# Kernel optimization log

Hardware: AMD Instinct MI355X
Metric: run time of the kernel (lower is better)

## Reference

```python
import jax, jax.numpy as jnp
import numpy as np

H, DK, DV, CHUNK = 4, 256, 256, 32

def _silu(x):
    return x * jax.nn.sigmoid(x)

def _l2norm(x, eps=1e-6):
    return x * jax.lax.rsqrt(jnp.sum(x * x, -1, keepdims=True) + eps)

def _rmsnorm(x, w, eps=1e-5):
    return x * jax.lax.rsqrt(jnp.mean(x * x, -1, keepdims=True) + eps) * w

def _causal_dwconv(x, w):
    # x: (B, L, C), w: (C, K) -> causal depthwise conv -> (B, L, C)
    C = x.shape[-1]
    K = w.shape[-1]
    xp = jnp.pad(x, ((0, 0), (K - 1, 0), (0, 0))).transpose(0, 2, 1)  # NCH
    y = jax.lax.conv_general_dilated(xp, w[:, None, :], (1,), 'VALID',
                                     feature_group_count=C,
                                     dimension_numbers=('NCH', 'OIH', 'NCH'))
    return y.transpose(0, 2, 1)

def _fir(x, filt):
    # x: (B, L, H, D), filt: (H, D, K) depthwise causal FIR per (head, channel)
    B, L, h, d = x.shape
    y = _causal_dwconv(x.reshape(B, L, h * d), filt.reshape(h * d, -1))
    return y.reshape(B, L, h, d)

def _delta_rule_chunkwise(q, k, v, beta):
    # q,k: (B,H,L,DK); v: (B,H,L,DV); beta: (B,H,L). L % CHUNK == 0.
    b, h, L, dk = q.shape
    dv = v.shape[-1]
    n = L // CHUNK
    q = _l2norm(q)
    k = _l2norm(k)
    v = v * beta[..., None]
    k_beta = k * beta[..., None]
    rs = lambda t: t.reshape(b, h, n, CHUNK, -1)
    q, k, v, k_beta = rs(q), rs(k), rs(v), rs(k_beta)
    eye = jnp.eye(CHUNK, dtype=q.dtype)
    strict_lower = jnp.tril(jnp.ones((CHUNK, CHUNK), bool), -1)
    A = jnp.where(strict_lower, jnp.einsum('bhncd,bhnsd->bhncs', k_beta, k), 0.0)
    # The torch row-wise loop computes (I + strict_lower(K_beta K^T))^{-1}
    attn_inv = jax.scipy.linalg.solve_triangular(eye + A, jnp.broadcast_to(eye, A.shape), lower=True)
    u = attn_inv @ v       # (b,h,n,c,dv)
    w = attn_inv @ k_beta  # (b,h,n,c,dk)
    incl_lower = jnp.tril(jnp.ones((CHUNK, CHUNK), bool))

    def step(S, inp):
        q_i, k_i, u_i, w_i = inp
        attn_local = jnp.where(incl_lower, q_i @ jnp.swapaxes(k_i, -1, -2), 0.0)
        u_t = u_i - w_i @ S
        o_i = q_i @ S + attn_local @ u_t
        return S + jnp.swapaxes(k_i, -1, -2) @ u_t, o_i

    S0 = jnp.zeros((b, h, dk, dv), q.dtype)
    xs = tuple(jnp.moveaxis(t, 2, 0) for t in (q, k, u, w))
    S, out = jax.lax.scan(step, S0, xs)
    return jnp.moveaxis(out, 0, 2).reshape(b, h, L, dv), S

def _stats(x):
    # per-branch head statistics over feature dim: mean, var, abs-mean, l2-norm
    return jnp.stack([x.mean(-1), x.var(-1), jnp.abs(x).mean(-1),
                      jnp.sqrt(jnp.sum(x * x, -1))], -1)

def _forward(x, Wq, Wk, Wv, Wb, conv_q, conv_k, conv_v, fir_long, fir_short,
             W1, b1, W2, b2, log_temp, base_bias, conv_residual_logit, rms_w, Wo):
    B, L, D = x.shape
    q = _silu(_causal_dwconv(x @ Wq, conv_q)).reshape(B, L, H, DK)
    k = _silu(_causal_dwconv(x @ Wk, conv_k)).reshape(B, L, H, DK)
    v = _silu(_causal_dwconv(x @ Wv, conv_v)).reshape(B, L, H, DV)
    beta = jax.nn.sigmoid(x @ Wb)  # (B, L, H)
    delta, _S = _delta_rule_chunkwise(q.transpose(0, 2, 1, 3), k.transpose(0, 2, 1, 3),
                                      v.transpose(0, 2, 1, 3), beta.transpose(0, 2, 1))
    delta = delta.transpose(0, 2, 1, 3)  # (B, L, H, DV)
    f_short = _fir(v, fir_short)
    f_long = _fir(v, fir_long)
    stats = jnp.concatenate([_stats(f_short), _stats(f_long), _stats(delta), _stats(v)], -1)
    hidden_exp = jnp.broadcast_to(x[:, :, None, :], (B, L, H, D))
    gate_in = jnp.concatenate([hidden_exp, stats], -1)  # (B,L,H,D+16)
    h1 = jax.nn.gelu(gate_in @ W1 + b1, approximate=False)
    logits = h1 @ W2 + b2 + base_bias  # (B, L, H, 4)
    temp = jax.nn.softplus(log_temp) + 1e-4
    p = jax.nn.softmax(logits / temp[:, None], -1)
    eps = 0.05  # step 0 -> alpha = 1 -> floor = floor_start
    p = jnp.maximum(p, jnp.array([eps, eps, 0.0, 0.0], p.dtype))
    p = p / jnp.sum(p, -1, keepdims=True)
    o = (p[..., 0:1] * f_short + p[..., 1:2] * f_long +
         p[..., 2:3] * delta + p[..., 3:4] * v)
    o = o + 0.5 * jax.nn.sigmoid(conv_residual_logit)[None, None, :, None] * f_short
    o = _rmsnorm(o, rms_w)
    return o.reshape(B, L, H * DV) @ Wo

def setup_inputs():
    key = jax.random.key(0)
    ks = jax.random.split(key, 13)
    B, L, D = 2, 2048, 1024
    f = jnp.float32
    n = lambda k, shape, s=0.02: jax.random.normal(k, shape, f) * s
    return {
        'x': jax.random.normal(ks[0], (B, L, D), f),
        'Wq': n(ks[1], (D, D)),
        'Wk': n(ks[2], (D, D)),
        'Wv': n(ks[3], (D, D)),
        'Wb': n(ks[4], (D, H)),
        'conv_q': n(ks[5], (D, 4), 0.1),
        'conv_k': n(ks[6], (D, 4), 0.1),
        'conv_v': n(ks[7], (D, 4), 0.1),
        'fir_long': n(ks[8], (H, DV, 64)),
        'fir_short': n(ks[9], (H, DV, 5)),
        'W1': n(ks[10], (D + 16, D)),
        'b1': jnp.zeros((D,), f),
        'W2': n(ks[11], (D, 4)),
        'b2': jnp.zeros((4,), f),
        'log_temp': jnp.full((H,), float(np.log(np.expm1(0.7))), f),
        'base_bias': jnp.tile(jnp.array([-0.5, -0.5, 1.0, 3.0], f), (H, 1)),
        'conv_residual_logit': jnp.full((H,), -2.0, f),
        'rms_w': jnp.ones((DV,), f),
        'Wo': n(ks[12], (D, D)),
    }

def reference(x, Wq, Wk, Wv, Wb, conv_q, conv_k, conv_v, fir_long, fir_short,
              W1, b1, W2, b2, log_temp, base_bias, conv_residual_logit, rms_w, Wo):
    return _forward(x, Wq, Wk, Wv, Wb, conv_q, conv_k, conv_v, fir_long, fir_short,
                    W1, b1, W2, b2, log_temp, base_bias, conv_residual_logit, rms_w, Wo)
```

## Files before the change

### kernel.cpp

```cpp
#include <hip/hip_runtime.h>
#include <math.h>

constexpr int NB = 2, NL = 2048, ND = 1024, NH = 4;
constexpr int NCHK = 64;
constexpr int NBL = NB * NL;
#define BLDSZ (NB * NL * ND)

constexpr int OPS_CH = 36864;
constexpr int STG_CH = 26624;

__device__ float g_q[BLDSZ];
__device__ float g_k[BLDSZ];
__device__ float g_v[BLDSZ];
__device__ float g_delta[BLDSZ];
__device__ float g_fs[BLDSZ];
__device__ float g_fl[BLDSZ];
__device__ float g_xw1[BLDSZ];
__device__ float g_beta[NBL * NH];
__device__ unsigned short g_ops[(size_t)8 * 64 * OPS_CH];
__device__ unsigned short g_xb[BLDSZ];
__device__ unsigned short g_omixb[BLDSZ];
__device__ unsigned short g_btw[5 * 1024 * 1024];

__device__ __forceinline__ float sigmoidf(float x) { return 1.f / (1.f + expf(-x)); }

__device__ __forceinline__ unsigned short f2bf(float f) {
  union { float f; unsigned int u; } v; v.f = f;
  unsigned int r = v.u + 0x7FFFu + ((v.u >> 16) & 1u);
  return (unsigned short)(r >> 16);
}
__device__ __forceinline__ float bf2f(unsigned int bits16) {
  union { unsigned int u; float f; } v; v.u = bits16 << 16; return v.f;
}
__device__ __forceinline__ unsigned int packbf(float a, float b) {
  return (unsigned int)f2bf(a) | ((unsigned int)f2bf(b) << 16);
}

typedef __attribute__((ext_vector_type(8))) short short8v;
typedef __attribute__((ext_vector_type(16))) float f32x16;

__device__ __forceinline__ unsigned int cvtpk(float lo, float hi) {
  unsigned int r;
  asm("v_cvt_pk_bf16_f32 %0, %1, %2" : "=v"(r) : "v"(lo), "v"(hi));
  return r;
}

__device__ __forceinline__ void mkfrag(const f32x16 v, short8v& fb0, short8v& fb1) {
  unsigned int P0 = cvtpk(v[0], v[1]),   P1 = cvtpk(v[2], v[3]);
  unsigned int P2 = cvtpk(v[4], v[5]),   P3 = cvtpk(v[6], v[7]);
  unsigned int P4 = cvtpk(v[8], v[9]),   P5 = cvtpk(v[10], v[11]);
  unsigned int P6 = cvtpk(v[12], v[13]), P7 = cvtpk(v[14], v[15]);
  asm("v_permlane32_swap_b32 %0, %1" : "+v"(P0), "+v"(P2));
  asm("v_permlane32_swap_b32 %0, %1" : "+v"(P1), "+v"(P3));
  asm("v_permlane32_swap_b32 %0, %1" : "+v"(P4), "+v"(P6));
  asm("v_permlane32_swap_b32 %0, %1" : "+v"(P5), "+v"(P7));
  unsigned int f0[4] = {P0, P1, P2, P3}, f1[4] = {P4, P5, P6, P7};
  fb0 = *(short8v*)f0; fb1 = *(short8v*)f1;
}

#define GLL16(SRC, DST)                                                                    \
  __builtin_amdgcn_global_load_lds(                                                        \
      (const __attribute__((address_space(1))) unsigned int*)(SRC),                        \
      (__attribute__((address_space(3))) unsigned int*)(DST), 16, 0, 0)

__device__ __forceinline__ void gemm128s(const unsigned short* __restrict__ A,
                                         const unsigned short* __restrict__ Bt,
                                         float* __restrict__ C, int m0, int n0, int t,
                                         unsigned short* As, unsigned short* Bs) {
  const int w = t >> 6, lane = t & 63, l31 = lane & 31, lhi = lane >> 5;
  const int wm = (w & 1) * 64, wn = (w >> 1) * 64;
  f32x16 acc[2][2];
#pragma unroll
  for (int mt = 0; mt < 2; ++mt)
#pragma unroll
    for (int nt = 0; nt < 2; ++nt)
#pragma unroll
      for (int e = 0; e < 16; ++e) acc[mt][nt][e] = 0.f;

  for (int k0 = 0; k0 < 1024; k0 += 32) {
    for (int sl = w; sl < 8; sl += 4) {
      int srow = sl * 16 + (lane >> 2);
      int gc = ((lane & 3) ^ (srow & 3)) * 8;
      GLL16(A + (size_t)(m0 + srow) * 1024 + k0 + gc, &As[sl * 512]);
      GLL16(Bt + (size_t)(n0 + srow) * 1024 + k0 + gc, &Bs[sl * 512]);
    }
    __syncthreads();
#pragma unroll
    for (int ksl = 0; ksl < 2; ++ksl) {
      int kb = ksl * 2 + lhi;
      short8v af[2], bf[2];
#pragma unroll
      for (int mt = 0; mt < 2; ++mt) {
        int row = wm + mt * 32 + l31;
        af[mt] = *(const short8v*)&As[row * 32 + ((kb ^ (row & 3)) * 8)];
      }
#pragma unroll
      for (int nt = 0; nt < 2; ++nt) {
        int row = wn + nt * 32 + l31;
        bf[nt] = *(const short8v*)&Bs[row * 32 + ((kb ^ (row & 3)) * 8)];
      }
#pragma unroll
      for (int mt = 0; mt < 2; ++mt)
#pragma unroll
        for (int nt = 0; nt < 2; ++nt)
          acc[mt][nt] = __builtin_amdgcn_mfma_f32_32x32x16_bf16(af[mt], bf[nt], acc[mt][nt], 0, 0, 0);
    }
    __syncthreads();
  }
#pragma unroll
  for (int mt = 0; mt < 2; ++mt)
#pragma unroll
    for (int nt = 0; nt < 2; ++nt) {
      int col = n0 + wn + nt * 32 + l31;
#pragma unroll
      for (int e = 0; e < 16; ++e) {
        int row = m0 + wm + mt * 32 + (e & 3) + 8 * (e >> 2) + 4 * lhi;
        C[(size_t)row * 1024 + col] = acc[mt][nt][e];
      }
    }
}

__global__ __launch_bounds__(256) void pack_all_kernel(const float* __restrict__ x,
                                                       const float* __restrict__ Wq,
                                                       const float* __restrict__ Wk,
                                                       const float* __restrict__ Wv,
                                                       const float* __restrict__ W1,
                                                       const float* __restrict__ Wo,
                                                       const float* __restrict__ Wb) {
  __shared__ float tile[64][65];
  int blk = blockIdx.x, t = threadIdx.x;
  if (blk < 2048) {
    int i8 = blk * 256 + t;
    const float* p = x + (size_t)i8 * 8;
    float4 a = *(const float4*)p;
    float4 b = *(const float4*)(p + 4);
    uint4 v;
    v.x = packbf(a.x, a.y); v.y = packbf(a.z, a.w);
    v.z = packbf(b.x, b.y); v.w = packbf(b.z, b.w);
    *(uint4*)&g_xb[(size_t)i8 * 8] = v;
    return;
  }
  if (blk < 3328) {
    int sel = (blk - 2048) >> 8, wb = (blk - 2048) & 255;
    const float* W = (sel == 0) ? Wq : (sel == 1) ? Wk : (sel == 2) ? Wv : (sel == 3) ? W1 : Wo;
    int bx = wb & 15, by = wb >> 4;
    int n0 = bx * 64, k0 = by * 64;
#pragma unroll
    for (int i = 0; i < 4; ++i) {
      int id = t + i * 256;
      int r = id >> 4, c4 = (id & 15) * 4;
      float4 v = *(const float4*)&W[(size_t)(k0 + r) * 1024 + n0 + c4];
      tile[r][c4 + 0] = v.x; tile[r][c4 + 1] = v.y; tile[r][c4 + 2] = v.z; tile[r][c4 + 3] = v.w;
    }
    __syncthreads();
    unsigned int* out = (unsigned int*)g_btw + (size_t)sel * 524288;
#pragma unroll
    for (int i = 0; i < 8; ++i) {
      int id = t + i * 256;
      int nn = id >> 5, ku = id & 31;
      out[(size_t)(n0 + nn) * 512 + (k0 >> 1) + ku] = packbf(tile[2 * ku][nn], tile[2 * ku + 1][nn]);
    }
    return;
  }
  int bl = blk - 3328;
  int h = t >> 6, lane = t & 63;
  const float* xr = x + (size_t)bl * ND;
  float acc = 0.f;
  for (int d = lane; d < ND; d += 64) acc += xr[d] * Wb[d * 4 + h];
#pragma unroll
  for (int off = 32; off; off >>= 1) acc += __shfl_xor(acc, off);
  if (lane == 0) g_beta[bl * 4 + h] = sigmoidf(acc);
}

__global__ __launch_bounds__(256, 3) void qkv_conv_kernel(const float* __restrict__ cq,
                                                          const float* __restrict__ ck,
                                                          const float* __restrict__ cv) {
  __shared__ unsigned short As[160 * 32];
  __shared__ unsigned short Bs[128 * 32];
  __shared__ unsigned short TF[131][132];
  const int sel = blockIdx.x >> 8, hb = blockIdx.x & 255;
  const unsigned short* A = g_xb;
  const unsigned short* Bt = g_btw + (size_t)sel * 1024 * 1024;
  const float* cw = (sel == 0) ? cq : (sel == 1) ? ck : cv;
  float* OUT = (sel == 0) ? g_q : (sel == 1) ? g_k : g_v;
  const int m0 = (hb >> 3) * 128, n0 = (hb & 7) * 128;
  const int t = threadIdx.x;
  const int w = t >> 6, lane = t & 63, l31 = lane & 31, lhi = lane >> 5;
  const int wm = (w & 1) * 64, wn = (w >> 1) * 64;

  f32x16 acc[2][2], acch;
#pragma unroll
  for (int mt = 0; mt < 2; ++mt)
#pragma unroll
    for (int nt = 0; nt < 2; ++nt)
#pragma unroll
      for (int e = 0; e < 16; ++e) acc[mt][nt][e] = 0.f;
#pragma unroll
  for (int e = 0; e < 16; ++e) acch[e] = 0.f;

  for (int k0 = 0; k0 < 1024; k0 += 32) {
    for (int sl = w; sl < 10; sl += 4) {
      int srow = sl * 16 + (lane >> 2);
      int gc = ((lane & 3) ^ (srow & 3)) * 8;
      int grow = m0 - 32 + srow;
      if (grow < 0) grow = 0;
      GLL16(A + (size_t)grow * 1024 + k0 + gc, &As[sl * 512]);
    }
    for (int sl = w; sl < 8; sl += 4) {
      int srow = sl * 16 + (lane >> 2);
      int gc = ((lane & 3) ^ (srow & 3)) * 8;
      GLL16(Bt + (size_t)(n0 + srow) * 1024 + k0 + gc, &Bs[sl * 512]);
    }
    __syncthreads();
#pragma unroll
    for (int ksl = 0; ksl < 2; ++ksl) {
      int kb = ksl * 2 + lhi;
      short8v af[2], bf[2], afh;
#pragma unroll
      for (int mt = 0; mt < 2; ++mt) {
        int row = 32 + wm + mt * 32 + l31;
        af[mt] = *(const short8v*)&As[row * 32 + ((kb ^ (row & 3)) * 8)];
      }
      {
        int row = l31;
        afh = *(const short8v*)&As[row * 32 + ((kb ^ (row & 3)) * 8)];
      }
#pragma unroll
      for (int nt = 0; nt < 2; ++nt) {
        int row = wn + nt * 32 + l31;
        bf[nt] = *(const short8v*)&Bs[row * 32 + ((kb ^ (row & 3)) * 8)];
      }
#pragma unroll
      for (int mt = 0; mt < 2; ++mt)
#pragma unroll
        for (int nt = 0; nt < 2; ++nt)
          acc[mt][nt] = __builtin_amdgcn_mfma_f32_32x32x16_bf16(af[mt], bf[nt], acc[mt][nt], 0, 0, 0);
      acch = __builtin_amdgcn_mfma_f32_32x32x16_bf16(afh, bf[w & 1], acch, 0, 0, 0);
    }
    __syncthreads();
  }

#pragma unroll
  for (int mt = 0; mt < 2; ++mt)
#pragma unroll
    for (int nt = 0; nt < 2; ++nt) {
      int tc = wn + nt * 32 + l31;
#pragma unroll
      for (int e = 0; e < 16; ++e) {
        int row_e = (e & 3) + 8 * (e >> 2) + 4 * lhi;
        TF[3 + wm + mt * 32 + row_e][tc] = f2bf(acc[mt][nt][e]);
      }
    }
#pragma unroll
  for (int e = 0; e < 16; ++e) {
    int row_e = (e & 3) + 8 * (e >> 2) + 4 * lhi;
    if (row_e >= 29) TF[row_e - 29][w * 32 + l31] = f2bf(acch[e]);
  }
  __syncthreads();

  {
    int c = t & 127;
    int rbase = (t >> 7) * 64;
    int ch = n0 + c;
    float w0 = cw[ch * 4 + 0], w1 = cw[ch * 4 + 1], w2 = cw[ch * 4 + 2], w3 = cw[ch * 4 + 3];
#pragma unroll 4
    for (int i = 0; i < 64; ++i) {
      int rr = rbase + i;
      int grow = m0 + rr;
      int l = grow & (NL - 1);
      float a = w3 * bf2f(TF[rr + 3][c]);
      if (l >= 1) a += w2 * bf2f(TF[rr + 2][c]);
      if (l >= 2) a += w1 * bf2f(TF[rr + 1][c]);
      if (l >= 3) a += w0 * bf2f(TF[rr + 0][c]);
      OUT[(size_t)grow * 1024 + ch] = a * sigmoidf(a);
    }
  }
}

__global__ __launch_bounds__(256) void hgemm_out_kernel(float* __restrict__ Cext) {
  __shared__ unsigned short As[128 * 32];
  __shared__ unsigned short Bs[128 * 32];
  gemm128s(g_omixb, g_btw + (size_t)4 * 1024 * 1024, Cext,
           (blockIdx.x >> 3) * 128, (blockIdx.x & 7) * 128, threadIdx.x, As, Bs);
}

__global__ __launch_bounds__(256) void delta_prep_kernel() {
  __shared__ float X[32][260];
  __shared__ float Y[32][260];
  __shared__ float Am[32][33];
  __shared__ float Tm[32][33];
  __shared__ float bet[32];
  int blk = blockIdx.x;
  int n = blk & 63, h = (blk >> 6) & 3, b = blk >> 8;
  int t = threadIdx.x;
  size_t rowbase = (size_t)(b * NL + n * 32);
  size_t obase = (size_t)blk * OPS_CH;
  const int st_ = t >> 5, j_ = (t >> 4) & 1, lh_ = (t >> 3) & 1, e_ = t & 7;
  const int l31_ = t & 31;

#pragma unroll
  for (int i = 0; i < 8; ++i) {
    int j = t + i * 256;
    int r = j >> 6, d4 = (j & 63) << 2;
    size_t gi = (rowbase + r) * ND + h * 256 + d4;
    *(float4*)&X[r][d4] = *(const float4*)&g_q[gi];
    *(float4*)&Y[r][d4] = *(const float4*)&g_k[gi];
  }
  if (t < 32) bet[t] = g_beta[(rowbase + t) * 4 + h];
  __syncthreads();

  {
    int wv = t >> 6, lane = t & 63;
    int r = wv * 8 + (lane >> 3), sub = lane & 7;
    float sq = 0.f, sk = 0.f;
#pragma unroll
    for (int m4 = 0; m4 < 8; ++m4) {
      float4 a = *(const float4*)&X[r][sub * 32 + m4 * 4];
      float4 bb = *(const float4*)&Y[r][sub * 32 + m4 * 4];
      sq += a.x * a.x + a.y * a.y + a.z * a.z + a.w * a.w;
      sk += bb.x * bb.x + bb.y * bb.y + bb.z * bb.z + bb.w * bb.w;
    }
    sq += __shfl_xor(sq, 1); sq += __shfl_xor(sq, 2); sq += __shfl_xor(sq, 4);
    sk += __shfl_xor(sk, 1); sk += __shfl_xor(sk, 2); sk += __shfl_xor(sk, 4);
    float rq = rsqrtf(sq + 1e-6f), rk = rsqrtf(sk + 1e-6f);
#pragma unroll
    for (int m4 = 0; m4 < 8; ++m4) {
      float4 a = *(const float4*)&X[r][sub * 32 + m4 * 4];
      a.x *= rq; a.y *= rq; a.z *= rq; a.w *= rq;
      *(float4*)&X[r][sub * 32 + m4 * 4] = a;
      float4 bb = *(const float4*)&Y[r][sub * 32 + m4 * 4];
      bb.x *= rk; bb.y *= rk; bb.z *= rk; bb.w *= rk;
      *(float4*)&Y[r][sub * 32 + m4 * 4] = bb;
    }
  }
  __syncthreads();

  if (t < 64) {
    const int al = t & 31, ah = t >> 5;
    f32x16 Cat;
#pragma unroll
    for (int e = 0; e < 16; ++e) Cat[e] = 0.f;
#pragma unroll
    for (int st = 0; st < 16; ++st) {
      int kb = st * 16 + ah * 8;
      float4 a0 = *(const float4*)&X[al][kb], a1 = *(const float4*)&X[al][kb + 4];
      float4 b0 = *(const float4*)&Y[al][kb], b1 = *(const float4*)&Y[al][kb + 4];
      unsigned int af[4] = {cvtpk(a0.x, a0.y), cvtpk(a0.z, a0.w), cvtpk(a1.x, a1.y), cvtpk(a1.z, a1.w)};
      unsigned int bf_[4] = {cvtpk(b0.x, b0.y), cvtpk(b0.z, b0.w), cvtpk(b1.x, b1.y), cvtpk(b1.z, b1.w)};
      Cat = __builtin_amdgcn_mfma_f32_32x32x16_bf16(*(short8v*)af, *(short8v*)bf_, Cat, 0, 0, 0);
    }
#pragma unroll
    for (int e = 0; e < 16; ++e) {
      int row = (e & 3) + 8 * (e >> 2) + 4 * ah, col = al;
      float v = (col <= row) ? Cat[e] : 0.f;
      g_ops[obase + 32768 + (size_t)(((col >> 4) * 64) + ((col >> 3) & 1) * 32 + row) * 8 + (col & 7)] = f2bf(v);
    }
  }

  {
    size_t qb = obase + 8192 + (size_t)(((st_ * 2 + j_) * 64) + lh_ * 32) * 8 + e_;
#pragma unroll 8
    for (int r = 0; r < 32; ++r)
      g_ops[qb + r * 8] = f2bf(X[r][t]);
#pragma unroll
    for (int j = 0; j < 2; ++j)
#pragma unroll
      for (int lh = 0; lh < 2; ++lh) {
        int kr0 = j * 16 + lh * 8;
        uint4 v;
        v.x = packbf(Y[kr0 + 0][t], Y[kr0 + 1][t]);
        v.y = packbf(Y[kr0 + 2][t], Y[kr0 + 3][t]);
        v.z = packbf(Y[kr0 + 4][t], Y[kr0 + 5][t]);
        v.w = packbf(Y[kr0 + 6][t], Y[kr0 + 7][t]);
        *(uint4*)&g_ops[obase + 16384 + (size_t)(((st_ * 2 + j) * 64) + lh * 32 + l31_) * 8] = v;
      }
  }
  __syncthreads();

#pragma unroll
  for (int i = 0; i < 8; ++i) {
    int j = t + i * 256;
    int r = j >> 6, d4 = (j & 63) << 2;
    float be = bet[r];
    float4 bb = *(const float4*)&Y[r][d4];
    bb.x *= be; bb.y *= be; bb.z *= be; bb.w *= be;
    *(float4*)&X[r][d4] = bb;
  }
  __syncthreads();

  if (t < 64) {
    const int al = t & 31, ah = t >> 5;
    f32x16 Cam;
#pragma unroll
    for (int e = 0; e < 16; ++e) Cam[e] = 0.f;
#pragma unroll
    for (int st = 0; st < 16; ++st) {
      int kb = st * 16 + ah * 8;
      float4 a0 = *(const float4*)&X[al][kb], a1 = *(const float4*)&X[al][kb + 4];
      float4 b0 = *(const float4*)&Y[al][kb], b1 = *(const float4*)&Y[al][kb + 4];
      unsigned int af[4] = {cvtpk(a0.x, a0.y), cvtpk(a0.z, a0.w), cvtpk(a1.x, a1.y), cvtpk(a1.z, a1.w)};
      unsigned int bf_[4] = {cvtpk(b0.x, b0.y), cvtpk(b0.z, b0.w), cvtpk(b1.x, b1.y), cvtpk(b1.z, b1.w)};
      Cam = __builtin_amdgcn_mfma_f32_32x32x16_bf16(*(short8v*)af, *(short8v*)bf_, Cam, 0, 0, 0);
    }
#pragma unroll
    for (int e = 0; e < 16; ++e) {
      int row = (e & 3) + 8 * (e >> 2) + 4 * ah, col = al;
      if (col < row) Am[row][col] = Cam[e];
    }
  }
  __syncthreads();

  if (t < 32) {
    int j = t;
    for (int i = 0; i < 32; ++i) {
      float a = (i == j) ? 1.f : 0.f;
      for (int m = j; m < i; ++m) a -= Am[i][m] * Tm[m][j];
      Tm[i][j] = a;
    }
  }
  __syncthreads();

  {
    float acc[32];
#pragma unroll
    for (int r = 0; r < 32; ++r) acc[r] = 0.f;
#pragma unroll
    for (int m = 0; m < 32; ++m) {
      float xv = X[m][t];
#pragma unroll
      for (int r = m; r < 32; ++r) acc[r] += Tm[r][m] * xv;
    }
    size_t wb = obase + (size_t)(((st_ * 2 + j_) * 64) + lh_ * 32) * 8 + e_;
#pragma unroll 8
    for (int r = 0; r < 32; ++r)
      g_ops[wb + r * 8] = f2bf(acc[r]);
  }
#pragma unroll
  for (int i = 0; i < 8; ++i) {
    int j = t + i * 256;
    int r = j >> 6, d4 = (j & 63) << 2;
    size_t gi = (rowbase + r) * ND + h * 256 + d4;
    float be = bet[r];
    float4 vv = *(const float4*)&g_v[gi];
    vv.x *= be; vv.y *= be; vv.z *= be; vv.w *= be;
    *(float4*)&Y[r][d4] = vv;
  }
  __syncthreads();

  {
    float acc[32];
#pragma unroll
    for (int r = 0; r < 32; ++r) acc[r] = 0.f;
#pragma unroll
    for (int m = 0; m < 32; ++m) {
      float yv = Y[m][t];
#pragma unroll
      for (int r = m; r < 32; ++r) acc[r] += Tm[r][m] * yv;
    }
    int q = t >> 5;
#pragma unroll
    for (int g = 0; g < 4; ++g)
#pragma unroll
      for (int lh = 0; lh < 2; ++lh) {
        int kr0 = 8 * g + 4 * lh;
        uint2 v;
        v.x = packbf(acc[kr0 + 0], acc[kr0 + 1]);
        v.y = packbf(acc[kr0 + 2], acc[kr0 + 3]);
        *(uint2*)&g_ops[obase + 24576 + (size_t)(((q * 4 + g) * 64) + lh * 32 + l31_) * 4] = v;
      }
  }
}

__global__ __launch_bounds__(256, 1) void scan_fir_kernel(const float* __restrict__ firl,
                                                          const float* __restrict__ firs) {
  __shared__ __align__(16) unsigned char smem[2 * STG_CH * 2];
  const int blk = blockIdx.x;
  const int t = threadIdx.x;

  if (blk < 64) {
    if (t >= 64) return;
    unsigned short (*buf)[STG_CH] = (unsigned short (*)[STG_CH])smem;
    const int bh = blk & 7;
    const int b = bh >> 2, h = bh & 3;
    const int s = blk >> 3;
    const int lane = t;
    const int l31 = lane & 31, lhi = lane >> 5;

    f32x16 Sacc[8];
#pragma unroll
    for (int st = 0; st < 8; ++st)
#pragma unroll
      for (int e = 0; e < 16; ++e) Sacc[st][e] = 0.f;

    const unsigned short* ops = g_ops + (size_t)bh * 64 * OPS_CH;
    const int fo = lane * 8;
    const int utg = 24576 + s * 1024;

#define STAGE_CHUNK(SRC, DST)                                                              \
    {                                                                                      \
      const unsigned short* sp = (SRC);                                                    \
      unsigned short* dp = (DST);                                                          \
      _Pragma("unroll")                                                                    \
      for (int k = 0; k < 48; ++k)                                                         \
        GLL16(sp + (size_t)k * 512 + fo, dp + k * 512);                                    \
      _Pragma("unroll")                                                                    \
      for (int k = 0; k < 2; ++k) {                                                        \
        GLL16(sp + utg + (size_t)k * 512 + fo, dp + 24576 + k * 512);                      \
        GLL16(sp + 32768 + (size_t)k * 512 + fo, dp + 25600 + k * 512);                    \
      }                                                                                    \
    }

    STAGE_CHUNK(ops, &buf[0][0]);

    for (int n = 0; n < 64; ++n) {
      const int cur = n & 1;
      if (n == 0) asm volatile("s_waitcnt vmcnt(0)" ::: "memory");
      else        asm volatile("s_waitcnt vmcnt(16)" ::: "memory");

      if (n < 63) STAGE_CHUNK(ops + (size_t)(n + 1) * OPS_CH, &buf[cur ^ 1][0]);

      const unsigned short* Lb = &buf[cur][0];
      f32x16 wuA, wuB, ooA, ooB;
#pragma unroll
      for (int e = 0; e < 16; ++e) { wuA[e] = 0.f; wuB[e] = 0.f; ooA[e] = 0.f; ooB[e] = 0.f; }

#pragma unroll
      for (int st = 0; st < 8; ++st) {
        short8v s0, s1;
        mkfrag(Sacc[st], s0, s1);
        short8v wa0 = *(const short8v*)&Lb[(st * 2 + 0) * 512 + fo];
        short8v wa1 = *(const short8v*)&Lb[(st * 2 + 1) * 512 + fo];
        short8v qa0 = *(const short8v*)&Lb[8192 + (st * 2 + 0) * 512 + fo];
        short8v qa1 = *(const short8v*)&Lb[8192 + (st * 2 + 1) * 512 + fo];
        wuA = __builtin_amdgcn_mfma_f32_32x32x16_bf16(wa0, s0, wuA, 0, 0, 0);
        wuB = __builtin_amdgcn_mfma_f32_32x32x16_bf16(wa1, s1, wuB, 0, 0, 0);
        ooA = __builtin_amdgcn_mfma_f32_32x32x16_bf16(qa0, s0, ooA, 0, 0, 0);
        ooB = __builtin_amdgcn_mfma_f32_32x32x16_bf16(qa1, s1, ooB, 0, 0, 0);
      }

      f32x16 ut;
#pragma unroll
      for (int g = 0; g < 4; ++g) {
        uint2 uu = *(const uint2*)&Lb[24576 + ((g * 64) + lhi * 32 + l31) * 4];
        ut[4 * g + 0] = bf2f(uu.x & 0xffffu) - wuA[4 * g + 0] - wuB[4 * g + 0];
        ut[4 * g + 1] = bf2f(uu.x >> 16)     - wuA[4 * g + 1] - wuB[4 * g + 1];
        ut[4 * g + 2] = bf2f(uu.y & 0xffffu) - wuA[4 * g + 2] - wuB[4 * g + 2];
        ut[4 * g + 3] = bf2f(uu.y >> 16)     - wuA[4 * g + 3] - wuB[4 * g + 3];
      }
      short8v u0, u1;
      mkfrag(ut, u0, u1);

      {
        short8v aa0 = *(const short8v*)&Lb[25600 + 0 * 512 + fo];
        short8v aa1 = *(const short8v*)&Lb[25600 + 1 * 512 + fo];
        ooA = __builtin_amdgcn_mfma_f32_32x32x16_bf16(aa0, u0, ooA, 0, 0, 0);
        ooB = __builtin_amdgcn_mfma_f32_32x32x16_bf16(aa1, u1, ooB, 0, 0, 0);
      }
#pragma unroll
      for (int st = 0; st < 8; ++st) {
        short8v ka0 = *(const short8v*)&Lb[16384 + (st * 2 + 0) * 512 + fo];
        short8v ka1 = *(const short8v*)&Lb[16384 + (st * 2 + 1) * 512 + fo];
        Sacc[st] = __builtin_amdgcn_mfma_f32_32x32x16_bf16(ka0, u0, Sacc[st], 0, 0, 0);
        Sacc[st] = __builtin_amdgcn_mfma_f32_32x32x16_bf16(ka1, u1, Sacc[st], 0, 0, 0);
      }

      size_t ob = ((size_t)(b * NL + n * 32)) * ND + h * 256 + s * 32 + l31;
#pragma unroll
      for (int e = 0; e < 16; ++e) {
        int row = (e & 3) + 8 * (e >> 2) + 4 * lhi;
        g_delta[ob + (size_t)row * ND] = ooA[e] + ooB[e];
      }
    }
#undef STAGE_CHUNK
  } else if (blk < 64 + 512) {
    float (*ft)[257] = (float (*)[257])smem;
    int fb_ = blk - 64;
    int cbk = fb_ & 3, lb = (fb_ >> 2) & 63, b = fb_ >> 8;
    int c = cbk * 256 + t;
    const float* fbp = firl + (size_t)cbk * 256 * 64;
#pragma unroll 4
    for (int i = 0; i < 64; ++i) {
      int j = t + i * 256;
      ft[j & 63][j >> 6] = fbp[j];
    }
    __syncthreads();
    float ff[64];
#pragma unroll
    for (int i = 0; i < 64; ++i) ff[i] = ft[i][t];
    float acc[32];
#pragma unroll
    for (int i = 0; i < 32; ++i) acc[i] = 0.f;
    const float* vb = g_v + (size_t)b * NL * ND + c;
    const int l0 = lb * 32;
#pragma unroll
    for (int d = 0; d < 95; ++d) {
      int lr = l0 - 63 + d;
      float vv = (lr >= 0) ? vb[(size_t)lr * ND] : 0.f;
      const int lo = (d > 63) ? (d - 63) : 0;
      const int hi = (d < 31) ? d : 31;
#pragma unroll
      for (int li = lo; li <= hi; ++li) acc[li] += ff[d - li] * vv;
    }
    float* ob = g_fl + ((size_t)(b * NL + l0)) * ND + c;
#pragma unroll
    for (int li = 0; li < 32; ++li) ob[(size_t)li * ND] = acc[li];
  } else if (blk < 64 + 512 + BLDSZ / 1024) {
    int idx4 = (blk - 576) * 256 + t;
    int c4 = idx4 & 255;
    int bl = idx4 >> 8;
    int l = bl & (NL - 1);
    float fw[4][5];
#pragma unroll
    for (int j = 0; j < 4; ++j)
#pragma unroll
      for (int tap = 0; tap < 5; ++tap) fw[j][tap] = firs[(c4 * 4 + j) * 5 + tap];
    float4 acc = {0.f, 0.f, 0.f, 0.f};
    const float4* v4 = (const float4*)g_v;
#pragma unroll
    for (int tap = 0; tap < 5; ++tap) {
      int ls = l + tap - 4;
      if (ls >= 0) {
        float4 vv = v4[(size_t)(bl + tap - 4) * 256 + c4];
        acc.x += fw[0][tap] * vv.x; acc.y += fw[1][tap] * vv.y;
        acc.z += fw[2][tap] * vv.z; acc.w += fw[3][tap] * vv.w;
      }
    }
    ((float4*)g_fs)[(size_t)bl * 256 + c4] = acc;
  } else {
    unsigned short* As = (unsigned short*)smem;
    unsigned short* Bs = (unsigned short*)smem + 4096;
    int hb = blk - (64 + 512 + BLDSZ / 1024);
    gemm128s(g_xb, g_btw + (size_t)3 * 1024 * 1024, g_xw1,
             (hb >> 3) * 128, (hb & 7) * 128, t, As, Bs);
  }
}

__global__ __launch_bounds__(256) void tail_kernel(const float* __restrict__ W1,
                                                   const float* __restrict__ b1,
                                                   const float* __restrict__ W2,
                                                   const float* __restrict__ b2,
                                                   const float* __restrict__ log_temp,
                                                   const float* __restrict__ base_bias,
                                                   const float* __restrict__ crl,
                                                   const float* __restrict__ rms_w) {
  __shared__ float st[4][16];
  __shared__ float red[4][4];
  __shared__ float pl[4][4];
  int bl = blockIdx.x, t = threadIdx.x;
  int h = t >> 6, lane = t & 63;

  {
    size_t base = (size_t)bl * ND + h * 256 + lane * 4;
#pragma unroll
    for (int br = 0; br < 4; ++br) {
      const float* p = (br == 0) ? g_fs : (br == 1) ? g_fl : (br == 2) ? g_delta : g_v;
      float4 x4 = *(const float4*)&p[base];
      float s = x4.x + x4.y + x4.z + x4.w;
      float s2 = x4.x * x4.x + x4.y * x4.y + x4.z * x4.z + x4.w * x4.w;
      float sa = fabsf(x4.x) + fabsf(x4.y) + fabsf(x4.z) + fabsf(x4.w);
#pragma unroll
      for (int off = 32; off; off >>= 1) {
        s += __shfl_xor(s, off);
        s2 += __shfl_xor(s2, off);
        sa += __shfl_xor(sa, off);
      }
      if (lane == 0) {
        float mean = s * (1.f / 256.f);
        st[h][br * 4 + 0] = mean;
        st[h][br * 4 + 1] = s2 * (1.f / 256.f) - mean * mean;
        st[h][br * 4 + 2] = sa * (1.f / 256.f);
        st[h][br * 4 + 3] = sqrtf(s2);
      }
    }
  }
  __syncthreads();

  const float* W1s = W1 + 1024 * 1024;
  for (int hh = 0; hh < 4; ++hh) {
    float sv[16];
#pragma unroll
    for (int s = 0; s < 16; ++s) sv[s] = st[hh][s];
    float a0 = 0.f, a1 = 0.f, a2 = 0.f, a3 = 0.f;
    for (int j = t; j < 1024; j += 256) {
      float val = g_xw1[(size_t)bl * 1024 + j] + b1[j];
#pragma unroll
      for (int s = 0; s < 16; ++s) val += sv[s] * W1s[s * 1024 + j];
      float gg = 0.5f * val * (1.f + erff(val * 0.70710678118654752f));
      float4 w2 = *(const float4*)&W2[j * 4];
      a0 += gg * w2.x; a1 += gg * w2.y; a2 += gg * w2.z; a3 += gg * w2.w;
    }
#pragma unroll
    for (int off = 32; off; off >>= 1) {
      a0 += __shfl_xor(a0, off); a1 += __shfl_xor(a1, off);
      a2 += __shfl_xor(a2, off); a3 += __shfl_xor(a3, off);
    }
    if (lane == 0) { red[h][0] = a0; red[h][1] = a1; red[h][2] = a2; red[h][3] = a3; }
    __syncthreads();
    if (t == 0) {
      float lg[4];
#pragma unroll
      for (int m = 0; m < 4; ++m)
        lg[m] = red[0][m] + red[1][m] + red[2][m] + red[3][m] + b2[m] + base_bias[hh * 4 + m];
      float lt = log_temp[hh];
      float sp = (lt > 20.f) ? lt : log1pf(expf(lt));
      float inv = 1.f / (sp + 1e-4f);
      float z0 = lg[0] * inv, z1 = lg[1] * inv, z2 = lg[2] * inv, z3 = lg[3] * inv;
      float mx = fmaxf(fmaxf(z0, z1), fmaxf(z2, z3));
      float e0 = expf(z0 - mx), e1 = expf(z1 - mx), e2 = expf(z2 - mx), e3 = expf(z3 - mx);
      float si = 1.f / (e0 + e1 + e2 + e3);
      float p0 = e0 * si, p1 = e1 * si, p2 = e2 * si, p3 = e3 * si;
      p0 = fmaxf(p0, 0.05f); p1 = fmaxf(p1, 0.05f);
      float s2i = 1.f / (p0 + p1 + p2 + p3);
      p0 *= s2i; p1 *= s2i; p2 *= s2i; p3 *= s2i;
      p0 += 0.5f * sigmoidf(crl[hh]);
      pl[hh][0] = p0; pl[hh][1] = p1; pl[hh][2] = p2; pl[hh][3] = p3;
    }
    __syncthreads();
  }

  float p0 = pl[h][0], p1 = pl[h][1], p2 = pl[h][2], p3 = pl[h][3];
  size_t base = (size_t)bl * ND + h * 256 + lane * 4;
  float4 a = *(const float4*)&g_fs[base];
  float4 bb = *(const float4*)&g_fl[base];
  float4 c = *(const float4*)&g_delta[base];
  float4 d = *(const float4*)&g_v[base];
  float o0 = p0 * a.x + p1 * bb.x + p2 * c.x + p3 * d.x;
  float o1 = p0 * a.y + p1 * bb.y + p2 * c.y + p3 * d.y;
  float o2 = p0 * a.z + p1 * bb.z + p2 * c.z + p3 * d.z;
  float o3 = p0 * a.w + p1 * bb.w + p2 * c.w + p3 * d.w;
  float s2 = o0 * o0 + o1 * o1 + o2 * o2 + o3 * o3;
#pragma unroll
  for (int off = 32; off; off >>= 1) s2 += __shfl_xor(s2, off);
  float rms = rsqrtf(s2 * (1.f / 256.f) + 1e-5f);
  float4 w4 = *(const float4*)&rms_w[lane * 4];
  uint2 pw;
  pw.x = packbf(o0 * rms * w4.x, o1 * rms * w4.y);
  pw.y = packbf(o2 * rms * w4.z, o3 * rms * w4.w);
  *(uint2*)&g_omixb[base] = pw;
}

extern "C" void kernel_launch(void* const* d_in, const int* in_sizes, int n_in,
                              void* d_out, int out_size, void* d_ws, size_t ws_size,
                              hipStream_t stream) {
  const float* x = (const float*)d_in[0];
  const float* Wq = (const float*)d_in[1];
  const float* Wk = (const float*)d_in[2];
  const float* Wv = (const float*)d_in[3];
  const float* Wb = (const float*)d_in[4];
  const float* cq = (const float*)d_in[5];
  const float* ck = (const float*)d_in[6];
  const float* cv = (const float*)d_in[7];
  const float* firl = (const float*)d_in[8];
  const float* firs = (const float*)d_in[9];
  const float* W1 = (const float*)d_in[10];
  const float* b1 = (const float*)d_in[11];
  const float* W2 = (const float*)d_in[12];
  const float* b2 = (const float*)d_in[13];
  const float* ltp = (const float*)d_in[14];
  const float* bbs = (const float*)d_in[15];
  const float* crl = (const float*)d_in[16];
  const float* rw = (const float*)d_in[17];
  const float* Wo = (const float*)d_in[18];
  float* out = (float*)d_out;

  dim3 blk(256);
  pack_all_kernel<<<2048 + 5 * 256 + NBL, blk, 0, stream>>>(x, Wq, Wk, Wv, W1, Wo, Wb);
  qkv_conv_kernel<<<768, blk, 0, stream>>>(cq, ck, cv);
  delta_prep_kernel<<<NB * NH * NCHK, blk, 0, stream>>>();
  scan_fir_kernel<<<64 + 512 + BLDSZ / 1024 + 256, blk, 0, stream>>>(firl, firs);
  tail_kernel<<<NBL, blk, 0, stream>>>(W1, b1, W2, b2, ltp, bbs, crl, rw);
  hgemm_out_kernel<<<256, blk, 0, stream>>>(out);
}
```

Baseline: 465.6 us.

## Split QKV GEMM from causal conv, drop LDS swizzle, unroll triangular solve

The fused QKV GEMM plus causal depthwise conv kernel is split in two. A plain GEMM writes bf16 intermediates to new global buffers, and a separate elementwise conv+SiLU kernel reads them back. The LDS XOR swizzle in the GEMM tile loads is removed in favour of linear layout, and the triangular-inverse loop is fully unrolled with predication. This drops the halo rows and the extra MFMA in the GEMM but adds a global round trip of three BLxD bf16 tensors, an extra launch, and possible LDS bank conflicts.

```diff
diff --git a/kernel.cpp b/kernel.cpp
--- a/kernel.cpp
+++ b/kernel.cpp
@@ -17,6 +17,9 @@
 __device__ float g_fl[BLDSZ];
 __device__ float g_xw1[BLDSZ];
 __device__ float g_beta[NBL * NH];
+__device__ unsigned short g_qlb[BLDSZ];
+__device__ unsigned short g_klb[BLDSZ];
+__device__ unsigned short g_vlb[BLDSZ];
 __device__ unsigned short g_ops[(size_t)8 * 64 * OPS_CH];
 __device__ unsigned short g_xb[BLDSZ];
 __device__ unsigned short g_omixb[BLDSZ];
@@ -63,10 +66,10 @@
       (const __attribute__((address_space(1))) unsigned int*)(SRC),                        \
       (__attribute__((address_space(3))) unsigned int*)(DST), 16, 0, 0)
 
-__device__ __forceinline__ void gemm128s(const unsigned short* __restrict__ A,
-                                         const unsigned short* __restrict__ Bt,
-                                         float* __restrict__ C, int m0, int n0, int t,
-                                         unsigned short* As, unsigned short* Bs) {
+__device__ __forceinline__ void gemm128(const unsigned short* __restrict__ A,
+                                        const unsigned short* __restrict__ Bt,
+                                        float* __restrict__ C, int m0, int n0, int t,
+                                        unsigned short* As, unsigned short* Bs) {
   const int w = t >> 6, lane = t & 63, l31 = lane & 31, lhi = lane >> 5;
   const int wm = (w & 1) * 64, wn = (w >> 1) * 64;
   f32x16 acc[2][2];
@@ -78,11 +81,13 @@
       for (int e = 0; e < 16; ++e) acc[mt][nt][e] = 0.f;
 
   for (int k0 = 0; k0 < 1024; k0 += 32) {
-    for (int sl = w; sl < 8; sl += 4) {
-      int srow = sl * 16 + (lane >> 2);
-      int gc = ((lane & 3) ^ (srow & 3)) * 8;
-      GLL16(A + (size_t)(m0 + srow) * 1024 + k0 + gc, &As[sl * 512]);
-      GLL16(Bt + (size_t)(n0 + srow) * 1024 + k0 + gc, &Bs[sl * 512]);
+#pragma unroll
+    for (int i = 0; i < 2; ++i) {
+      int s0 = i * 256 + w * 64;
+      int sl = s0 + lane;
+      int srow = sl >> 2, skb = sl & 3;
+      GLL16(A + (size_t)(m0 + srow) * 1024 + k0 + skb * 8, &As[s0 * 8]);
+      GLL16(Bt + (size_t)(n0 + srow) * 1024 + k0 + skb * 8, &Bs[s0 * 8]);
     }
     __syncthreads();
 #pragma unroll
@@ -92,12 +97,12 @@
 #pragma unroll
       for (int mt = 0; mt < 2; ++mt) {
         int row = wm + mt * 32 + l31;
-        af[mt] = *(const short8v*)&As[row * 32 + ((kb ^ (row & 3)) * 8)];
+        af[mt] = *(const short8v*)&As[row * 32 + kb * 8];
       }
 #pragma unroll
       for (int nt = 0; nt < 2; ++nt) {
         int row = wn + nt * 32 + l31;
-        bf[nt] = *(const short8v*)&Bs[row * 32 + ((kb ^ (row & 3)) * 8)];
+        bf[nt] = *(const short8v*)&Bs[row * 32 + kb * 8];
       }
 #pragma unroll
       for (int mt = 0; mt < 2; ++mt)
@@ -172,116 +177,95 @@
   if (lane == 0) g_beta[bl * 4 + h] = sigmoidf(acc);
 }
 
-__global__ __launch_bounds__(256, 3) void qkv_conv_kernel(const float* __restrict__ cq,
-                                                          const float* __restrict__ ck,
-                                                          const float* __restrict__ cv) {
-  __shared__ unsigned short As[160 * 32];
+__global__ __launch_bounds__(256) void qkv_gemm_kernel() {
+  __shared__ unsigned short As[128 * 32];
   __shared__ unsigned short Bs[128 * 32];
-  __shared__ unsigned short TF[131][132];
   const int sel = blockIdx.x >> 8, hb = blockIdx.x & 255;
   const unsigned short* A = g_xb;
   const unsigned short* Bt = g_btw + (size_t)sel * 1024 * 1024;
-  const float* cw = (sel == 0) ? cq : (sel == 1) ? ck : cv;
-  float* OUT = (sel == 0) ? g_q : (sel == 1) ? g_k : g_v;
+  unsigned short* C = (sel == 0) ? g_qlb : (sel == 1) ? g_klb : g_vlb;
   const int m0 = (hb >> 3) * 128, n0 = (hb & 7) * 128;
   const int t = threadIdx.x;
   const int w = t >> 6, lane = t & 63, l31 = lane & 31, lhi = lane >> 5;
   const int wm = (w & 1) * 64, wn = (w >> 1) * 64;
-
-  f32x16 acc[2][2], acch;
+  f32x16 acc[2][2];
 #pragma unroll
   for (int mt = 0; mt < 2; ++mt)
 #pragma unroll
     for (int nt = 0; nt < 2; ++nt)
 #pragma unroll
       for (int e = 0; e < 16; ++e) acc[mt][nt][e] = 0.f;
-#pragma unroll
-  for (int e = 0; e < 16; ++e) acch[e] = 0.f;
 
   for (int k0 = 0; k0 < 1024; k0 += 32) {
-    for (int sl = w; sl < 10; sl += 4) {
-      int srow = sl * 16 + (lane >> 2);
-      int gc = ((lane & 3) ^ (srow & 3)) * 8;
-      int grow = m0 - 32 + srow;
-      if (grow < 0) grow = 0;
-      GLL16(A + (size_t)grow * 1024 + k0 + gc, &As[sl * 512]);
-    }
-    for (int sl = w; sl < 8; sl += 4) {
-      int srow = sl * 16 + (lane >> 2);
-      int gc = ((lane & 3) ^ (srow & 3)) * 8;
-      GLL16(Bt + (size_t)(n0 + srow) * 1024 + k0 + gc, &Bs[sl * 512]);
+#pragma unroll
+    for (int i = 0; i < 2; ++i) {
+      int s0 = i * 256 + w * 64;
+      int sl = s0 + lane;
+      int srow = sl >> 2, skb = sl & 3;
+      GLL16(A + (size_t)(m0 + srow) * 1024 + k0 + skb * 8, &As[s0 * 8]);
+      GLL16(Bt + (size_t)(n0 + srow) * 1024 + k0 + skb * 8, &Bs[s0 * 8]);
     }
     __syncthreads();
 #pragma unroll
     for (int ksl = 0; ksl < 2; ++ksl) {
       int kb = ksl * 2 + lhi;
-      short8v af[2], bf[2], afh;
+      short8v af[2], bf[2];
 #pragma unroll
       for (int mt = 0; mt < 2; ++mt) {
-        int row = 32 + wm + mt * 32 + l31;
-        af[mt] = *(const short8v*)&As[row * 32 + ((kb ^ (row & 3)) * 8)];
-      }
-      {
-        int row = l31;
-        afh = *(const short8v*)&As[row * 32 + ((kb ^ (row & 3)) * 8)];
+        int row = wm + mt * 32 + l31;
+        af[mt] = *(const short8v*)&As[row * 32 + kb * 8];
       }
 #pragma unroll
       for (int nt = 0; nt < 2; ++nt) {
         int row = wn + nt * 32 + l31;
-        bf[nt] = *(const short8v*)&Bs[row * 32 + ((kb ^ (row & 3)) * 8)];
+        bf[nt] = *(const short8v*)&Bs[row * 32 + kb * 8];
       }
 #pragma unroll
       for (int mt = 0; mt < 2; ++mt)
 #pragma unroll
         for (int nt = 0; nt < 2; ++nt)
           acc[mt][nt] = __builtin_amdgcn_mfma_f32_32x32x16_bf16(af[mt], bf[nt], acc[mt][nt], 0, 0, 0);
-      acch = __builtin_amdgcn_mfma_f32_32x32x16_bf16(afh, bf[w & 1], acch, 0, 0, 0);
     }
     __syncthreads();
   }
-
 #pragma unroll
   for (int mt = 0; mt < 2; ++mt)
 #pragma unroll
     for (int nt = 0; nt < 2; ++nt) {
-      int tc = wn + nt * 32 + l31;
+      int col = n0 + wn + nt * 32 + l31;
 #pragma unroll
       for (int e = 0; e < 16; ++e) {
-        int row_e = (e & 3) + 8 * (e >> 2) + 4 * lhi;
-        TF[3 + wm + mt * 32 + row_e][tc] = f2bf(acc[mt][nt][e]);
-      }
-    }
-#pragma unroll
-  for (int e = 0; e < 16; ++e) {
-    int row_e = (e & 3) + 8 * (e >> 2) + 4 * lhi;
-    if (row_e >= 29) TF[row_e - 29][w * 32 + l31] = f2bf(acch[e]);
-  }
-  __syncthreads();
-
-  {
-    int c = t & 127;
-    int rbase = (t >> 7) * 64;
-    int ch = n0 + c;
-    float w0 = cw[ch * 4 + 0], w1 = cw[ch * 4 + 1], w2 = cw[ch * 4 + 2], w3 = cw[ch * 4 + 3];
-#pragma unroll 4
-    for (int i = 0; i < 64; ++i) {
-      int rr = rbase + i;
-      int grow = m0 + rr;
-      int l = grow & (NL - 1);
-      float a = w3 * bf2f(TF[rr + 3][c]);
-      if (l >= 1) a += w2 * bf2f(TF[rr + 2][c]);
-      if (l >= 2) a += w1 * bf2f(TF[rr + 1][c]);
-      if (l >= 3) a += w0 * bf2f(TF[rr + 0][c]);
-      OUT[(size_t)grow * 1024 + ch] = a * sigmoidf(a);
-    }
-  }
+        int row = m0 + wm + mt * 32 + (e & 3) + 8 * (e >> 2) + 4 * lhi;
+        C[(size_t)row * 1024 + col] = f2bf(acc[mt][nt][e]);
+      }
+    }
+}
+
+__global__ __launch_bounds__(256) void conv3_kernel(const float* __restrict__ cq,
+                                                    const float* __restrict__ ck,
+                                                    const float* __restrict__ cv) {
+  int blk = blockIdx.x, t = threadIdx.x;
+  int sel = blk >> 14;
+  const float* cw = (sel == 0) ? cq : (sel == 1) ? ck : cv;
+  const unsigned short* in = (sel == 0) ? g_qlb : (sel == 1) ? g_klb : g_vlb;
+  float* out = (sel == 0) ? g_q : (sel == 1) ? g_k : g_v;
+  int idx = (blk & 16383) * 256 + t;
+  int c = idx & (ND - 1);
+  int bl = idx >> 10;
+  int l = bl & (NL - 1);
+  float w0 = cw[c * 4 + 0], w1 = cw[c * 4 + 1], w2 = cw[c * 4 + 2], w3 = cw[c * 4 + 3];
+  float acc = w3 * bf2f(in[(size_t)bl * ND + c]);
+  if (l >= 1) acc += w2 * bf2f(in[(size_t)(bl - 1) * ND + c]);
+  if (l >= 2) acc += w1 * bf2f(in[(size_t)(bl - 2) * ND + c]);
+  if (l >= 3) acc += w0 * bf2f(in[(size_t)(bl - 3) * ND + c]);
+  out[idx] = acc * sigmoidf(acc);
 }
 
 __global__ __launch_bounds__(256) void hgemm_out_kernel(float* __restrict__ Cext) {
   __shared__ unsigned short As[128 * 32];
   __shared__ unsigned short Bs[128 * 32];
-  gemm128s(g_omixb, g_btw + (size_t)4 * 1024 * 1024, Cext,
-           (blockIdx.x >> 3) * 128, (blockIdx.x & 7) * 128, threadIdx.x, As, Bs);
+  gemm128(g_omixb, g_btw + (size_t)4 * 1024 * 1024, Cext,
+          (blockIdx.x >> 3) * 128, (blockIdx.x & 7) * 128, threadIdx.x, As, Bs);
 }
 
 __global__ __launch_bounds__(256) void delta_prep_kernel() {
@@ -411,10 +395,15 @@
   __syncthreads();
 
   if (t < 32) {
-    int j = t;
+    const int j = t;
+#pragma unroll
     for (int i = 0; i < 32; ++i) {
       float a = (i == j) ? 1.f : 0.f;
-      for (int m = j; m < i; ++m) a -= Am[i][m] * Tm[m][j];
+#pragma unroll
+      for (int m = 0; m < i; ++m) {
+        float p = Am[i][m] * Tm[m][j];
+        a -= (m >= j) ? p : 0.f;
+      }
       Tm[i][j] = a;
     }
   }
@@ -630,8 +619,8 @@
     unsigned short* As = (unsigned short*)smem;
     unsigned short* Bs = (unsigned short*)smem + 4096;
     int hb = blk - (64 + 512 + BLDSZ / 1024);
-    gemm128s(g_xb, g_btw + (size_t)3 * 1024 * 1024, g_xw1,
-             (hb >> 3) * 128, (hb & 7) * 128, t, As, Bs);
+    gemm128(g_xb, g_btw + (size_t)3 * 1024 * 1024, g_xw1,
+            (hb >> 3) * 128, (hb & 7) * 128, t, As, Bs);
   }
 }
 
@@ -765,7 +754,8 @@
 
   dim3 blk(256);
   pack_all_kernel<<<2048 + 5 * 256 + NBL, blk, 0, stream>>>(x, Wq, Wk, Wv, W1, Wo, Wb);
-  qkv_conv_kernel<<<768, blk, 0, stream>>>(cq, ck, cv);
+  qkv_gemm_kernel<<<768, blk, 0, stream>>>();
+  conv3_kernel<<<3 * 16384, blk, 0, stream>>>(cq, ck, cv);
   delta_prep_kernel<<<NB * NH * NCHK, blk, 0, stream>>>();
   scan_fir_kernel<<<64 + 512 + BLDSZ / 1024 + 256, blk, 0, stream>>>(firl, firs);
   tail_kernel<<<NBL, blk, 0, stream>>>(W1, b1, W2, b2, ltp, bbs, crl, rw);
```

Measured after the change: 438.4 us. -5.8%, faster.
